# Optimization experiments

Measured on AMD Instinct MI355X. Metric: run time of the kernel, lower is better.

Reference implementation:

```python
import jax, jax.numpy as jnp
import numpy as np

H = 32  # hidden_layer_size

def setup_inputs() -> dict:
    key = jax.random.key(0)
    ks = jax.random.split(key, 12)
    B, T, I = 4096, 512, 1
    x = jax.random.normal(ks[0], (B, T, I), dtype=jnp.float32)
    # linear_1: input_size -> H
    W1 = jax.random.normal(ks[1], (H, I), dtype=jnp.float32) * (1.0 / np.sqrt(I))
    b1 = jnp.zeros((H,), dtype=jnp.float32)
    # LSTM layer 0 (input H) and layer 1 (input H); torch gate order i,f,g,o
    Wih0 = jax.random.normal(ks[2], (4 * H, H), dtype=jnp.float32) * np.sqrt(2.0 / H)  # kaiming
    Whh0 = jax.random.normal(ks[3], (4 * H, H), dtype=jnp.float32) * (1.0 / np.sqrt(H))
    bih0 = jnp.zeros((4 * H,), dtype=jnp.float32)
    bhh0 = jnp.zeros((4 * H,), dtype=jnp.float32)
    Wih1 = jax.random.normal(ks[4], (4 * H, H), dtype=jnp.float32) * np.sqrt(2.0 / H)
    Whh1 = jax.random.normal(ks[5], (4 * H, H), dtype=jnp.float32) * (1.0 / np.sqrt(H))
    bih1 = jnp.zeros((4 * H,), dtype=jnp.float32)
    bhh1 = jnp.zeros((4 * H,), dtype=jnp.float32)
    # linear_2: num_layers*H -> 1
    W2 = jax.random.normal(ks[6], (1, 2 * H), dtype=jnp.float32) * (1.0 / np.sqrt(2 * H))
    b2 = jnp.zeros((1,), dtype=jnp.float32)
    return {"x": x, "W1": W1, "b1": b1,
            "Wih0": Wih0, "Whh0": Whh0, "bih0": bih0, "bhh0": bhh0,
            "Wih1": Wih1, "Whh1": Whh1, "bih1": bih1, "bhh1": bhh1,
            "W2": W2, "b2": b2}


def _lstm_layer(inp, Wih, Whh, bih, bhh):
    # inp: [B, T, H_in]; returns (ys [B, T, H], h_final [B, H])
    B = inp.shape[0]
    # precompute input-to-gate projections for all timesteps (one big GEMM)
    pre = jnp.einsum('bti,gi->tbg', inp, Wih) + (bih + bhh)  # [T, B, 4H]

    def step(carry, p_t):
        h, c = carry
        z = p_t + h @ Whh.T  # [B, 4H]
        i, f, g, o = jnp.split(z, 4, axis=-1)
        i = jax.nn.sigmoid(i)
        f = jax.nn.sigmoid(f)
        g = jnp.tanh(g)
        o = jax.nn.sigmoid(o)
        c = f * c + i * g
        h = o * jnp.tanh(c)
        return (h, c), h

    h0 = jnp.zeros((B, H), dtype=inp.dtype)
    c0 = jnp.zeros((B, H), dtype=inp.dtype)
    (h_f, _), ys = jax.lax.scan(step, (h0, c0), pre)
    return jnp.transpose(ys, (1, 0, 2)), h_f


def reference(x, W1, b1, Wih0, Whh0, bih0, bhh0, Wih1, Whh1, bih1, bhh1, W2, b2):
    # linear_1 + ReLU
    h = jax.nn.relu(jnp.einsum('bti,oi->bto', x, W1) + b1)  # [B, T, H]
    y0, hf0 = _lstm_layer(h, Wih0, Whh0, bih0, bhh0)
    _, hf1 = _lstm_layer(y0, Wih1, Whh1, bih1, bhh1)
    # h_n.permute(1,0,2).reshape(B, -1) -> concat layer finals along feature dim
    hcat = jnp.concatenate([hf0, hf1], axis=-1)  # [B, 2H]
    # dropout: eval mode (identity)
    preds = hcat @ W2.T + b2  # [B, 1]
    return preds[:, -1]  # [B]
```

## Files before the change

### kernel.cpp

```cpp
#include <hip/hip_runtime.h>

#define HH 32
#define NB 16
#define NT 512
#define TT 512

typedef float f32x4 __attribute__((ext_vector_type(4)));
typedef __bf16 bf16x8 __attribute__((ext_vector_type(8)));
typedef unsigned int u32;
typedef unsigned short u16;
typedef u32 u32x4 __attribute__((ext_vector_type(4)));

#if __has_builtin(__builtin_amdgcn_exp2f)
#define EXP2F(x) __builtin_amdgcn_exp2f(x)
#else
#define EXP2F(x) exp2f(x)
#endif
#if __has_builtin(__builtin_amdgcn_rcpf)
#define RCPF(x) __builtin_amdgcn_rcpf(x)
#else
#define RCPF(x) (1.0f / (x))
#endif

#define S_SIGM (-1.44269504f)
#define S_TANH (-2.88539008f)

static __device__ __forceinline__ f32x4 mfma16(bf16x8 a, bf16x8 b, f32x4 c) {
  return __builtin_amdgcn_mfma_f32_16x16x32_bf16(a, b, c, 0, 0, 0);
}

static __device__ __forceinline__ u32 rne_hi(u32 b) {
  return (b + 0x7FFFu + ((b >> 16) & 1u)) & 0xFFFF0000u;
}
static __device__ __forceinline__ u32 pack_hi16(u32 a, u32 b) {
#if __has_builtin(__builtin_amdgcn_perm)
  return __builtin_amdgcn_perm(a, b, 0x03020706u);
#else
  return (b & 0xFFFF0000u) | (a >> 16);
#endif
}
static __device__ __forceinline__ u32 pack_hl(float h) {
  const u32 b = __builtin_bit_cast(u32, h);
  const u32 r = rne_hi(b);
  const float lo = h - __builtin_bit_cast(float, r);
  return pack_hi16(r, __builtin_bit_cast(u32, lo));
}

static __device__ __forceinline__ bf16x8 load_wfrag_ph(const float* __restrict__ M,
                                                       int tile, int half, int lane) {
  const int m = lane & 15;
  const int q = m & 3;
  const int gi = q * HH + 4 * tile + (m >> 2);
  const int kappa = lane >> 4;
  const float s = (q == 2) ? S_TANH : S_SIGM;
  const float* p = M + gi * HH + 16 * half + 4 * kappa;
  u32x4 hw;
#pragma unroll
  for (int i = 0; i < 4; ++i) {
    const float v = p[i] * s;
    const u32 w16 = rne_hi(__builtin_bit_cast(u32, v)) >> 16;
    hw[i] = w16 | (w16 << 16);
  }
  return __builtin_bit_cast(bf16x8, hw);
}

__global__ void __launch_bounds__(NT)
lstm_fused_v6(const float* __restrict__ x,
              const float* __restrict__ W1, const float* __restrict__ b1,
              const float* __restrict__ Wih0, const float* __restrict__ Whh0,
              const float* __restrict__ bih0, const float* __restrict__ bhh0,
              const float* __restrict__ Wih1, const float* __restrict__ Whh1,
              const float* __restrict__ bih1, const float* __restrict__ bhh1,
              const float* __restrict__ W2, const float* __restrict__ b2,
              float* __restrict__ out, int T)
{
  __shared__ __align__(16) u32 h0P[2][2][256];
  __shared__ __align__(16) u32 h1P[2][2][256];
  __shared__ __align__(16) u32 hxP[2][2][256];
  __shared__ __align__(16) float xT[TT * NB];

  const int tid  = threadIdx.x;
  const int lane = tid & 63;
  const int wS   = __builtin_amdgcn_readfirstlane(tid >> 6);
  const bool isL0 = (wS < 4);
  const int tq   = wS & 3;
  const int kap  = lane >> 4;
  const int b    = lane & 15;
  const int b0   = blockIdx.x * NB;

  const float* Wr   = isL0 ? Whh0 : Whh1;
  const float* Wi_  = isL0 ? Wih0 : Wih1;
  const float* bihp = isL0 ? bih0 : bih1;
  const float* bhhp = isL0 ? bhh0 : bhh1;

  const bf16x8 wrA0 = load_wfrag_ph(Wr,  tq,     0, lane);
  const bf16x8 wrA1 = load_wfrag_ph(Wr,  tq,     1, lane);
  const bf16x8 wiA0 = load_wfrag_ph(Wi_, tq,     0, lane);
  const bf16x8 wiA1 = load_wfrag_ph(Wi_, tq,     1, lane);
  const bf16x8 wrB0 = load_wfrag_ph(Wr,  tq + 4, 0, lane);
  const bf16x8 wrB1 = load_wfrag_ph(Wr,  tq + 4, 1, lane);
  const bf16x8 wiB0 = load_wfrag_ph(Wi_, tq + 4, 0, lane);
  const bf16x8 wiB1 = load_wfrag_ph(Wi_, tq + 4, 1, lane);

  const int uA = 4 * tq + kap;
  const int uB = uA + 16;
  f32x4 biasA, biasB;
#pragma unroll
  for (int q = 0; q < 4; ++q) {
    const float s = (q == 2) ? S_TANH : S_SIGM;
    biasA[q] = (bihp[q * HH + uA] + bhhp[q * HH + uA]) * s;
    biasB[q] = (bihp[q * HH + uB] + bhhp[q * HH + uB]) * s;
  }
  const int slot = tq * 64 + b * 4 + kap;
  const int frd  = lane * 8;

  const float W1a = W1[uA], b1a = b1[uA];
  const float W1b = W1[uB], b1b = b1[uB];
  const int   w2o = isL0 ? 0 : HH;
  const float W2a = W2[w2o + uA], W2b = W2[w2o + uB];

  {
    const int row  = tid & 15;
    const int cbase = (tid >> 4) * 16;
    if (cbase + 16 <= T) {
      const float* xp = x + (size_t)(b0 + row) * T + cbase;
#pragma unroll
      for (int j = 0; j < 16; j += 4) {
        const float4 v = *(const float4*)(xp + j);
        xT[(cbase + j + 0) * NB + row] = v.x;
        xT[(cbase + j + 1) * NB + row] = v.y;
        xT[(cbase + j + 2) * NB + row] = v.z;
        xT[(cbase + j + 3) * NB + row] = v.w;
      }
    }
  }
  ((u32*)h0P)[tid] = 0; ((u32*)h0P)[tid + 512] = 0;
  ((u32*)h1P)[tid] = 0; ((u32*)h1P)[tid + 512] = 0;
  ((u32*)hxP)[tid] = 0; ((u32*)hxP)[tid + 512] = 0;
  __syncthreads();

  if (isL0) {
    const float xv = xT[b];
    hxP[0][0][slot] = pack_hl(fmaxf(__builtin_fmaf(xv, W1a, b1a), 0.0f));
    hxP[0][1][slot] = pack_hl(fmaxf(__builtin_fmaf(xv, W1b, b1b), 0.0f));
  }
  float cA = 0.0f, cB = 0.0f, hA = 0.0f, hB = 0.0f;
  __syncthreads();

#define GATES(z, c, h) {                                                \
    const float ei = EXP2F(z[0]), ef = EXP2F(z[1]);                     \
    const float eg = EXP2F(z[2]), eo = EXP2F(z[3]);                     \
    const float iv = RCPF(1.0f + ei), fv = RCPF(1.0f + ef);             \
    const float gv = __builtin_fmaf(2.0f, RCPF(1.0f + eg), -1.0f);      \
    const float ov = RCPF(1.0f + eo);                                   \
    c = __builtin_fmaf(fv, c, iv * gv);                                 \
    h = ov * __builtin_fmaf(2.0f, RCPF(1.0f + EXP2F(c * S_TANH)), -1.0f); \
  }

#define STEP(kk, WB, DO_L0, DO_L1, DO_HIN)                              \
  {                                                                     \
    const int RB = (WB) ^ 1;                                            \
    if (isL0) {                                                         \
      if (DO_L0) {                                                      \
        const bf16x8 S0 = *(const bf16x8*)((const u16*)h0P[RB][0] + frd); \
        const bf16x8 S1 = *(const bf16x8*)((const u16*)h0P[RB][1] + frd); \
        const bf16x8 P0 = *(const bf16x8*)((const u16*)hxP[WB][0] + frd); \
        const bf16x8 P1 = *(const bf16x8*)((const u16*)hxP[WB][1] + frd); \
        f32x4 zA = mfma16(wiA1, P1, biasA);                             \
        f32x4 zB = mfma16(wiB1, P1, biasB);                             \
        zA = mfma16(wiA0, P0, zA);  zB = mfma16(wiB0, P0, zB);          \
        zA = mfma16(wrA1, S1, zA);  zB = mfma16(wrB1, S1, zB);          \
        zA = mfma16(wrA0, S0, zA);  zB = mfma16(wrB0, S0, zB);          \
        if (DO_HIN) {                                                   \
          const float xv = xT[((kk) + 1) * NB + b];                     \
          hxP[RB][0][slot] =                                            \
              pack_hl(fmaxf(__builtin_fmaf(xv, W1a, b1a), 0.0f));       \
          hxP[RB][1][slot] =                                            \
              pack_hl(fmaxf(__builtin_fmaf(xv, W1b, b1b), 0.0f));       \
        }                                                               \
        GATES(zA, cA, hA);                                              \
        GATES(zB, cB, hB);                                              \
        h0P[WB][0][slot] = pack_hl(hA);                                 \
        h0P[WB][1][slot] = pack_hl(hB);                                 \
      }                                                                 \
    } else {                                                            \
      if (DO_L1) {                                                      \
        const bf16x8 S0 = *(const bf16x8*)((const u16*)h1P[WB][0] + frd); \
        const bf16x8 S1 = *(const bf16x8*)((const u16*)h1P[WB][1] + frd); \
        const bf16x8 P0 = *(const bf16x8*)((const u16*)h0P[RB][0] + frd); \
        const bf16x8 P1 = *(const bf16x8*)((const u16*)h0P[RB][1] + frd); \
        f32x4 zA = mfma16(wiA1, P1, biasA);                             \
        f32x4 zB = mfma16(wiB1, P1, biasB);                             \
        zA = mfma16(wiA0, P0, zA);  zB = mfma16(wiB0, P0, zB);          \
        zA = mfma16(wrA1, S1, zA);  zB = mfma16(wrB1, S1, zB);          \
        zA = mfma16(wrA0, S0, zA);  zB = mfma16(wrB0, S0, zB);          \
        GATES(zA, cA, hA);                                              \
        GATES(zB, cB, hB);                                              \
        h1P[RB][0][slot] = pack_hl(hA);                                 \
        h1P[RB][1][slot] = pack_hl(hB);                                 \
      }                                                                 \
    }                                                                   \
    __syncthreads();                                                    \
  }

  STEP(0, 0, true, false, true);
  for (int kk = 1; kk + 1 < T; kk += 2) {
    STEP(kk, 1, true, true, true);
    STEP(kk + 1, 0, true, true, true);
  }
  STEP(T - 1, 1, true, true, false);
  STEP(T, 0, false, true, false);

#undef STEP
#undef GATES

  xT[(wS * 4 + kap) * NB + b] = __builtin_fmaf(hA, W2a, hB * W2b);
  __syncthreads();
  if (tid < NB) {
    float acc = b2[0];
#pragma unroll
    for (int j = 0; j < 32; ++j) acc += xT[j * NB + tid];
    out[b0 + tid] = acc;
  }
}

extern "C" void kernel_launch(void* const* d_in, const int* in_sizes, int n_in,
                              void* d_out, int out_size, void* d_ws, size_t ws_size,
                              hipStream_t stream) {
  const float* x    = (const float*)d_in[0];
  const float* W1   = (const float*)d_in[1];
  const float* b1   = (const float*)d_in[2];
  const float* Wih0 = (const float*)d_in[3];
  const float* Whh0 = (const float*)d_in[4];
  const float* bih0 = (const float*)d_in[5];
  const float* bhh0 = (const float*)d_in[6];
  const float* Wih1 = (const float*)d_in[7];
  const float* Whh1 = (const float*)d_in[8];
  const float* bih1 = (const float*)d_in[9];
  const float* bhh1 = (const float*)d_in[10];
  const float* W2   = (const float*)d_in[11];
  const float* b2   = (const float*)d_in[12];

  const int B = out_size;
  const int I = in_sizes[1] / HH;
  const int T = in_sizes[0] / (B * I);
  const int blocks = B / NB;

  lstm_fused_v6<<<blocks, NT, 0, stream>>>(
      x, W1, b1, Wih0, Whh0, bih0, bhh0, Wih1, Whh1, bih1, bhh1, W2, b2,
      (float*)d_out, T);
}
```

Before: 232.4 us.

## Split LSTM work so every wave computes both layers for one hidden tile

Instead of dedicating four waves to layer 0 and four to layer 1, each of the 8 waves now handles one 4-unit tile of hidden state for both layers, running layer 0 then layer 1 within the same step. This balances the per-step work across waves and shares the h0 fragment loads between the layer-0 recurrent input and the layer-1 input. Each wave now issues two serial gate computations per step instead of two parallel tiles per layer, which changes the dependency chain length and instruction mix per step.

```diff
diff --git a/kernel.cpp b/kernel.cpp
--- a/kernel.cpp
+++ b/kernel.cpp
@@ -65,7 +65,7 @@
 }
 
 __global__ void __launch_bounds__(NT)
-lstm_fused_v6(const float* __restrict__ x,
+lstm_fused_v7(const float* __restrict__ x,
               const float* __restrict__ W1, const float* __restrict__ b1,
               const float* __restrict__ Wih0, const float* __restrict__ Whh0,
               const float* __restrict__ bih0, const float* __restrict__ bhh0,
@@ -81,46 +81,38 @@
 
   const int tid  = threadIdx.x;
   const int lane = tid & 63;
-  const int wS   = __builtin_amdgcn_readfirstlane(tid >> 6);
-  const bool isL0 = (wS < 4);
-  const int tq   = wS & 3;
-  const int kap  = lane >> 4;
+  const int w    = tid >> 6;
+  const int G    = lane >> 4;
   const int b    = lane & 15;
   const int b0   = blockIdx.x * NB;
 
-  const float* Wr   = isL0 ? Whh0 : Whh1;
-  const float* Wi_  = isL0 ? Wih0 : Wih1;
-  const float* bihp = isL0 ? bih0 : bih1;
-  const float* bhhp = isL0 ? bhh0 : bhh1;
-
-  const bf16x8 wrA0 = load_wfrag_ph(Wr,  tq,     0, lane);
-  const bf16x8 wrA1 = load_wfrag_ph(Wr,  tq,     1, lane);
-  const bf16x8 wiA0 = load_wfrag_ph(Wi_, tq,     0, lane);
-  const bf16x8 wiA1 = load_wfrag_ph(Wi_, tq,     1, lane);
-  const bf16x8 wrB0 = load_wfrag_ph(Wr,  tq + 4, 0, lane);
-  const bf16x8 wrB1 = load_wfrag_ph(Wr,  tq + 4, 1, lane);
-  const bf16x8 wiB0 = load_wfrag_ph(Wi_, tq + 4, 0, lane);
-  const bf16x8 wiB1 = load_wfrag_ph(Wi_, tq + 4, 1, lane);
-
-  const int uA = 4 * tq + kap;
-  const int uB = uA + 16;
-  f32x4 biasA, biasB;
+  const bf16x8 wr00 = load_wfrag_ph(Whh0, w, 0, lane);
+  const bf16x8 wr01 = load_wfrag_ph(Whh0, w, 1, lane);
+  const bf16x8 wi00 = load_wfrag_ph(Wih0, w, 0, lane);
+  const bf16x8 wi01 = load_wfrag_ph(Wih0, w, 1, lane);
+  const bf16x8 wr10 = load_wfrag_ph(Whh1, w, 0, lane);
+  const bf16x8 wr11 = load_wfrag_ph(Whh1, w, 1, lane);
+  const bf16x8 wi10 = load_wfrag_ph(Wih1, w, 0, lane);
+  const bf16x8 wi11 = load_wfrag_ph(Wih1, w, 1, lane);
+
+  const int uu = 4 * w + G;
+  f32x4 bias0, bias1;
 #pragma unroll
   for (int q = 0; q < 4; ++q) {
     const float s = (q == 2) ? S_TANH : S_SIGM;
-    biasA[q] = (bihp[q * HH + uA] + bhhp[q * HH + uA]) * s;
-    biasB[q] = (bihp[q * HH + uB] + bhhp[q * HH + uB]) * s;
-  }
-  const int slot = tq * 64 + b * 4 + kap;
+    bias0[q] = (bih0[q * HH + uu] + bhh0[q * HH + uu]) * s;
+    bias1[q] = (bih1[q * HH + uu] + bhh1[q * HH + uu]) * s;
+  }
+
+  const int half = uu >> 4;
+  const int slot = ((uu & 15) >> 2) * 64 + b * 4 + (uu & 3);
   const int frd  = lane * 8;
 
-  const float W1a = W1[uA], b1a = b1[uA];
-  const float W1b = W1[uB], b1b = b1[uB];
-  const int   w2o = isL0 ? 0 : HH;
-  const float W2a = W2[w2o + uA], W2b = W2[w2o + uB];
+  const float W1u = W1[uu], b1u = b1[uu];
+  const float W2a = W2[uu], W2b = W2[HH + uu];
 
   {
-    const int row  = tid & 15;
+    const int row   = tid & 15;
     const int cbase = (tid >> 4) * 16;
     if (cbase + 16 <= T) {
       const float* xp = x + (size_t)(b0 + row) * T + cbase;
@@ -139,12 +131,11 @@
   ((u32*)hxP)[tid] = 0; ((u32*)hxP)[tid + 512] = 0;
   __syncthreads();
 
-  if (isL0) {
+  {
     const float xv = xT[b];
-    hxP[0][0][slot] = pack_hl(fmaxf(__builtin_fmaf(xv, W1a, b1a), 0.0f));
-    hxP[0][1][slot] = pack_hl(fmaxf(__builtin_fmaf(xv, W1b, b1b), 0.0f));
-  }
-  float cA = 0.0f, cB = 0.0f, hA = 0.0f, hB = 0.0f;
+    hxP[0][half][slot] = pack_hl(fmaxf(__builtin_fmaf(xv, W1u, b1u), 0.0f));
+  }
+  float c0 = 0.0f, c1 = 0.0f, h0v = 0.0f, h1v = 0.0f;
   __syncthreads();
 
 #define GATES(z, c, h) {                                                \
@@ -157,50 +148,37 @@
     h = ov * __builtin_fmaf(2.0f, RCPF(1.0f + EXP2F(c * S_TANH)), -1.0f); \
   }
 
-#define STEP(kk, WB, DO_L0, DO_L1, DO_HIN)                              \
-  {                                                                     \
-    const int RB = (WB) ^ 1;                                            \
-    if (isL0) {                                                         \
-      if (DO_L0) {                                                      \
-        const bf16x8 S0 = *(const bf16x8*)((const u16*)h0P[RB][0] + frd); \
-        const bf16x8 S1 = *(const bf16x8*)((const u16*)h0P[RB][1] + frd); \
-        const bf16x8 P0 = *(const bf16x8*)((const u16*)hxP[WB][0] + frd); \
-        const bf16x8 P1 = *(const bf16x8*)((const u16*)hxP[WB][1] + frd); \
-        f32x4 zA = mfma16(wiA1, P1, biasA);                             \
-        f32x4 zB = mfma16(wiB1, P1, biasB);                             \
-        zA = mfma16(wiA0, P0, zA);  zB = mfma16(wiB0, P0, zB);          \
-        zA = mfma16(wrA1, S1, zA);  zB = mfma16(wrB1, S1, zB);          \
-        zA = mfma16(wrA0, S0, zA);  zB = mfma16(wrB0, S0, zB);          \
-        if (DO_HIN) {                                                   \
-          const float xv = xT[((kk) + 1) * NB + b];                     \
-          hxP[RB][0][slot] =                                            \
-              pack_hl(fmaxf(__builtin_fmaf(xv, W1a, b1a), 0.0f));       \
-          hxP[RB][1][slot] =                                            \
-              pack_hl(fmaxf(__builtin_fmaf(xv, W1b, b1b), 0.0f));       \
-        }                                                               \
-        GATES(zA, cA, hA);                                              \
-        GATES(zB, cB, hB);                                              \
-        h0P[WB][0][slot] = pack_hl(hA);                                 \
-        h0P[WB][1][slot] = pack_hl(hB);                                 \
-      }                                                                 \
-    } else {                                                            \
-      if (DO_L1) {                                                      \
-        const bf16x8 S0 = *(const bf16x8*)((const u16*)h1P[WB][0] + frd); \
-        const bf16x8 S1 = *(const bf16x8*)((const u16*)h1P[WB][1] + frd); \
-        const bf16x8 P0 = *(const bf16x8*)((const u16*)h0P[RB][0] + frd); \
-        const bf16x8 P1 = *(const bf16x8*)((const u16*)h0P[RB][1] + frd); \
-        f32x4 zA = mfma16(wiA1, P1, biasA);                             \
-        f32x4 zB = mfma16(wiB1, P1, biasB);                             \
-        zA = mfma16(wiA0, P0, zA);  zB = mfma16(wiB0, P0, zB);          \
-        zA = mfma16(wrA1, S1, zA);  zB = mfma16(wrB1, S1, zB);          \
-        zA = mfma16(wrA0, S0, zA);  zB = mfma16(wrB0, S0, zB);          \
-        GATES(zA, cA, hA);                                              \
-        GATES(zB, cB, hB);                                              \
-        h1P[RB][0][slot] = pack_hl(hA);                                 \
-        h1P[RB][1][slot] = pack_hl(hB);                                 \
-      }                                                                 \
-    }                                                                   \
-    __syncthreads();                                                    \
+#define STEP(kk, WB, DO_L0, DO_L1, DO_HIN)                               \
+  {                                                                      \
+    const int RB = (WB) ^ 1;                                             \
+    const bf16x8 S0 = *(const bf16x8*)((const u16*)h0P[RB][0] + frd);    \
+    const bf16x8 S1 = *(const bf16x8*)((const u16*)h0P[RB][1] + frd);    \
+    if (DO_L0) {                                                         \
+      const bf16x8 P0 = *(const bf16x8*)((const u16*)hxP[WB][0] + frd);  \
+      const bf16x8 P1 = *(const bf16x8*)((const u16*)hxP[WB][1] + frd);  \
+      f32x4 z0 = mfma16(wi01, P1, bias0);                                \
+      z0 = mfma16(wi00, P0, z0);                                         \
+      z0 = mfma16(wr01, S1, z0);                                         \
+      z0 = mfma16(wr00, S0, z0);                                         \
+      if (DO_HIN) {                                                      \
+        const float xv = xT[((kk) + 1) * NB + b];                        \
+        hxP[RB][half][slot] =                                            \
+            pack_hl(fmaxf(__builtin_fmaf(xv, W1u, b1u), 0.0f));          \
+      }                                                                  \
+      GATES(z0, c0, h0v);                                                \
+      h0P[WB][half][slot] = pack_hl(h0v);                                \
+    }                                                                    \
+    if (DO_L1) {                                                         \
+      const bf16x8 T0 = *(const bf16x8*)((const u16*)h1P[WB][0] + frd);  \
+      const bf16x8 T1 = *(const bf16x8*)((const u16*)h1P[WB][1] + frd);  \
+      f32x4 z1 = mfma16(wi11, S1, bias1);                                \
+      z1 = mfma16(wi10, S0, z1);                                         \
+      z1 = mfma16(wr11, T1, z1);                                         \
+      z1 = mfma16(wr10, T0, z1);                                         \
+      GATES(z1, c1, h1v);                                                \
+      h1P[RB][half][slot] = pack_hl(h1v);                                \
+    }                                                                    \
+    __syncthreads();                                                     \
   }
 
   STEP(0, 0, true, false, true);
@@ -214,12 +192,12 @@
 #undef STEP
 #undef GATES
 
-  xT[(wS * 4 + kap) * NB + b] = __builtin_fmaf(hA, W2a, hB * W2b);
+  xT[uu * NB + b] = __builtin_fmaf(h0v, W2a, h1v * W2b);
   __syncthreads();
   if (tid < NB) {
     float acc = b2[0];
 #pragma unroll
-    for (int j = 0; j < 32; ++j) acc += xT[j * NB + tid];
+    for (int u = 0; u < HH; ++u) acc += xT[u * NB + tid];
     out[b0 + tid] = acc;
   }
 }
@@ -246,7 +224,7 @@
   const int T = in_sizes[0] / (B * I);
   const int blocks = B / NB;
 
-  lstm_fused_v6<<<blocks, NT, 0, stream>>>(
+  lstm_fused_v7<<<blocks, NT, 0, stream>>>(
       x, W1, b1, Wih0, Whh0, bih0, bhh0, Wih1, Whh1, bih1, bhh1, W2, b2,
       (float*)d_out, T);
 }
```

Measured after the change: 228.4 us, median of 2. Within noise of the previous version (-1.7%).
